# Kernel optimization log

Hardware: AMD Instinct MI355X
Metric: run time of the kernel (lower is better)

## Reference

```python
import jax, jax.numpy as jnp
import numpy as np

B, S = 1, 2048
D = 2048            # n_embd
H = 16              # num heads
KV = 4              # num kv heads
GROUPS = H // KV
D_NOPE = 128
D_ROPE = 64
D_QK = D_NOPE + D_ROPE   # 192
D_V = 128
Q_RANK = 1536
KV_RANK = 512
EPS = 1e-6
MAX_POS = 4096


def rms_norm(x, w, eps=EPS):
    x32 = x.astype(jnp.float32)
    y = x32 * jax.lax.rsqrt(jnp.mean(x32 * x32, axis=-1, keepdims=True) + eps)
    return y.astype(x.dtype) * w


def rotate_half(x):
    x1, x2 = jnp.split(x, 2, axis=-1)
    return jnp.concatenate((-x2, x1), axis=-1)


def setup_inputs() -> dict:
    key = jax.random.key(0)
    ks = jax.random.split(key, 10)
    inv_freq = 1.0 / (10000.0 ** (jnp.arange(0, D_ROPE, 2, dtype=jnp.float32) / D_ROPE))
    t = jnp.arange(MAX_POS, dtype=jnp.float32)
    freqs = jnp.outer(t, inv_freq)                      # [MAX_POS, D_ROPE//2]
    emb = jnp.concatenate((freqs, freqs), axis=-1)      # [MAX_POS, D_ROPE]
    def lin(k, fan_in, fan_out):
        return jax.random.normal(k, (fan_in, fan_out), dtype=jnp.float32) * (fan_in ** -0.5)
    return {
        "hidden_states": jax.random.normal(ks[0], (B, S, D), dtype=jnp.float32),
        "cos": jnp.cos(emb)[None],                      # [1, MAX_POS, D_ROPE]
        "sin": jnp.sin(emb)[None],
        "wq_a": lin(ks[1], D, Q_RANK),
        "q_a_ln_w": jnp.ones((Q_RANK,), jnp.float32),
        "wq_b": lin(ks[2], Q_RANK, H * D_QK),
        "wkv_a": lin(ks[3], D, KV_RANK + D_ROPE),
        "kv_a_ln_w": jnp.ones((KV_RANK,), jnp.float32),
        "wkv_b": lin(ks[4], KV_RANK, KV * (D_NOPE + D_V)),
        "wo": lin(ks[5], H * D_V, D),
        "cache_position": jnp.arange(S, dtype=jnp.int64),
    }


def reference(hidden_states, cos, sin, wq_a, q_a_ln_w, wq_b, wkv_a, kv_a_ln_w,
              wkv_b, wo, cache_position):
    b, s, _ = hidden_states.shape
    # --- query low-rank path ---
    q_a = hidden_states @ wq_a                           # [B,S,Q_RANK]
    q = rms_norm(q_a, q_a_ln_w) @ wq_b                   # [B,S,H*D_QK]
    q = q.reshape(b, s, H, D_QK).transpose(0, 2, 1, 3)   # [B,H,S,D_QK]
    q_pass, q_rot = q[..., :D_NOPE], q[..., D_NOPE:]
    # --- kv low-rank path ---
    ckv = hidden_states @ wkv_a                          # [B,S,KV_RANK+D_ROPE]
    k_pass_a, k_rot_a = ckv[..., :KV_RANK], ckv[..., KV_RANK:]
    kv = rms_norm(k_pass_a, kv_a_ln_w) @ wkv_b           # [B,S,KV*(D_NOPE+D_V)]
    kv = kv.reshape(b, s, KV, D_NOPE + D_V).transpose(0, 2, 1, 3)  # [B,KV,S,*]
    k_pass, v = kv[..., :D_NOPE], kv[..., D_NOPE:]
    # --- partial RoPE ---
    c = cos[0][cache_position][None, None]               # [1,1,S,D_ROPE]
    sn = sin[0][cache_position][None, None]
    q_rot = q_rot * c + rotate_half(q_rot) * sn          # [B,H,S,D_ROPE]
    k_rot = k_rot_a[:, None]                             # [B,1,S,D_ROPE]
    k_rot = k_rot * c + rotate_half(k_rot) * sn
    k_rot = jnp.broadcast_to(k_rot, (b, KV, s, D_ROPE))
    k = jnp.concatenate((k_pass, k_rot), axis=-1)        # [B,KV,S,D_QK]
    # GQA expansion (repeat_interleave over head dim)
    k = jnp.repeat(k, GROUPS, axis=1)                    # [B,H,S,D_QK]
    v = jnp.repeat(v, GROUPS, axis=1)                    # [B,H,S,D_V]
    q_full = jnp.concatenate((q_pass, q_rot), axis=-1)   # [B,H,S,D_QK]
    # causal SDPA (default scale = 1/sqrt(D_QK), matching torch sdpa)
    scale = 1.0 / jnp.sqrt(jnp.float32(D_QK))
    scores = jnp.einsum("bhqd,bhkd->bhqk", q_full, k) * scale
    causal = jnp.tril(jnp.ones((s, s), dtype=bool))
    scores = jnp.where(causal[None, None], scores, jnp.finfo(scores.dtype).min)
    attn = jax.nn.softmax(scores, axis=-1)
    out = jnp.einsum("bhqk,bhkd->bhqd", attn, v)         # [B,H,S,D_V]
    out = out.transpose(0, 2, 1, 3).reshape(b, s, H * D_V)
    return out @ wo                                      # [B,S,D]
```

## Files before the change

kernel.cpp:

```cpp
#include <hip/hip_runtime.h>
#include <hip/hip_bf16.h>


#define S_LEN 2048
#define D_MODEL 2048
#define NH 16
#define NKV 4
#define D_QK 192
#define D_NOPE 128
#define D_ROPE 64
#define D_V 128
#define Q_RANK 1536
#define KV_RANK 512
#define CKV_PITCH 640
#define QDIM (NH * D_QK)
#define KVDIM (NKV * (D_NOPE + D_V))
#define ODIM (NH * D_V)
#define SCALE_QK 0.07216878364870322f
#define SPLIT 2

#define DT_B16 0
#define DT_F32 1
#define DT_AUTO 2

typedef __bf16 bf16x8 __attribute__((ext_vector_type(8)));
typedef float  f32x4  __attribute__((ext_vector_type(4)));
typedef unsigned short u16x8 __attribute__((ext_vector_type(8)));

typedef __attribute__((address_space(1))) const unsigned int as1_u32;
typedef __attribute__((address_space(3))) unsigned int as3_u32;

__device__ __forceinline__ void gl2lds16(const unsigned short* g, unsigned short* l) {
    __builtin_amdgcn_global_load_lds((as1_u32*)g, (as3_u32*)l, 16, 0, 0);
}

__device__ __forceinline__ float b2f(unsigned short u) {
    return __uint_as_float(((unsigned int)u) << 16);
}
__device__ __forceinline__ unsigned short f2b(float f) {
    unsigned int u = __float_as_uint(f);
    return (unsigned short)((u + 0x7fffu + ((u >> 16) & 1u)) >> 16);
}
__device__ __forceinline__ bool flag_f32(const unsigned* dt) {
    return dt[0] == 0x3F800000u;
}
__device__ __forceinline__ bool eff_f32(int mode, bool f32) {
    return mode == DT_F32 || (mode == DT_AUTO && f32);
}
__device__ __forceinline__ float ldany(const void* p, size_t i, bool f32) {
    return f32 ? ((const float*)p)[i] : b2f(((const unsigned short*)p)[i]);
}

__device__ __forceinline__ int xcd_swz(int id, int nwg) {
    return (id & 7) * (nwg >> 3) + (id >> 3);
}

#if __has_builtin(__builtin_amdgcn_mov_dpp)
#define ROR16F(x, n) __int_as_float(__builtin_amdgcn_mov_dpp(__float_as_int(x), 0x120 + (n), 0xf, 0xf, true))
#else
#define ROR16F(x, n) __shfl_xor((x), (n))
#endif

__global__ void __launch_bounds__(256)
prep_k(const void* __restrict__ hs, unsigned short* __restrict__ hsb,
       const void* __restrict__ wq_a, unsigned short* __restrict__ wqaT,
       const void* __restrict__ wkv_a, unsigned short* __restrict__ wkvaT,
       const void* __restrict__ wq_b, unsigned short* __restrict__ wqbT,
       const void* __restrict__ wkv_b, unsigned short* __restrict__ wkvbT,
       const void* __restrict__ wo, unsigned short* __restrict__ woT,
       const unsigned* __restrict__ dt)
{
    const bool f32 = flag_f32(dt);
    const int t = threadIdx.x;
    int id = blockIdx.x;

    if (id < 1024) {
        const int base = id * 4096;
        for (int i = t; i < 4096; i += 256)
            hsb[base + i] = f2b(ldany(hs, base + i, f32));
        return;
    }
    id -= 1024;

    const void* W; unsigned short* WT; int Kdim, Ncols, nkb;
    if (id < 768)        { W = wq_a;  WT = wqaT;  Kdim = D_MODEL; Ncols = Q_RANK;           nkb = 32; }
    else if (id < 1088)  { id -= 768;  W = wkv_a; WT = wkvaT; Kdim = D_MODEL; Ncols = KV_RANK + D_ROPE; nkb = 32; }
    else if (id < 2240)  { id -= 1088; W = wq_b;  WT = wqbT;  Kdim = Q_RANK;  Ncols = QDIM;  nkb = 24; }
    else if (id < 2368)  { id -= 2240; W = wkv_b; WT = wkvbT; Kdim = KV_RANK; Ncols = KVDIM; nkb = 8;  }
    else                 { id -= 2368; W = wo;    WT = woT;   Kdim = ODIM;    Ncols = D_MODEL; nkb = 32; }

    const int k0 = (id % nkb) * 64, n0 = (id / nkb) * 64;

    __shared__ unsigned short tile[64][65];
    for (int i = t; i < 4096; i += 256) {
        int r = i >> 6, c = i & 63;
        float v = (n0 + c < Ncols) ? ldany(W, (size_t)(k0 + r) * Ncols + n0 + c, f32) : 0.f;
        tile[c][r] = f2b(v);
    }
    __syncthreads();
    for (int i = t; i < 4096; i += 256) {
        int nn = i >> 6, kk = i & 63;
        WT[(size_t)(n0 + nn) * Kdim + k0 + kk] = tile[nn][kk];
    }
}

#define SM(BUF, MAT, SUB) (smem + (((BUF) * 4 + (MAT) * 2 + (SUB)) * 4096))

__device__ __forceinline__ void
gemm_core(unsigned short* smem,
          const unsigned short* __restrict__ A, int lda,
          const unsigned short* __restrict__ BT, int ldb, int colB,
          void* __restrict__ C, int ldc, int colC, int K, bool cf, int row0)
{
    const int t = threadIdx.x;
    const int w = t >> 6, lane = t & 63;
    const int half = w >> 2;
    const int wq = w & 3;
    const int wr = wq & 1, wc = wq >> 1;
    const int n = lane & 15, quad = lane >> 4;
    const int e0 = t * 8;
    const int er = e0 >> 5, ec = e0 & 31;

    f32x4 acc[4][4];
#pragma unroll
    for (int i = 0; i < 4; ++i)
#pragma unroll
        for (int j = 0; j < 4; ++j) acc[i][j] = (f32x4){0.f, 0.f, 0.f, 0.f};

#define STAGE(BUF, KB)                                                         \
    do {                                                                       \
        gl2lds16(A  + (size_t)(row0 + er) * lda + (KB) + ec,                   \
                 SM(BUF, 0, 0) + e0);                                          \
        gl2lds16(A  + (size_t)(row0 + er) * lda + (KB) + 32 + ec,              \
                 SM(BUF, 0, 1) + e0);                                          \
        gl2lds16(BT + (size_t)(colB + er) * ldb + (KB) + ec,                   \
                 SM(BUF, 1, 0) + e0);                                          \
        gl2lds16(BT + (size_t)(colB + er) * ldb + (KB) + 32 + ec,              \
                 SM(BUF, 1, 1) + e0);                                          \
    } while (0)

    STAGE(0, 0);

    int cur = 0;
    for (int k0 = 0; k0 < K; k0 += 64) {
        __syncthreads();

        if (k0 + 64 < K) STAGE(cur ^ 1, k0 + 64);

        const unsigned short* Asub = SM(cur, 0, half);
        const unsigned short* Bsub = SM(cur, 1, half);

        bf16x8 af[4], bfr[4];
#pragma unroll
        for (int i = 0; i < 4; ++i)
            af[i] = *(const bf16x8*)&Asub[(wr * 64 + i * 16 + n) * 32 + quad * 8];
#pragma unroll
        for (int j = 0; j < 4; ++j)
            bfr[j] = *(const bf16x8*)&Bsub[(wc * 64 + j * 16 + n) * 32 + quad * 8];
#pragma unroll
        for (int i = 0; i < 4; ++i)
#pragma unroll
            for (int j = 0; j < 4; ++j)
                acc[i][j] = __builtin_amdgcn_mfma_f32_16x16x32_bf16(af[i], bfr[j], acc[i][j], 0, 0, 0);

        cur ^= 1;
    }
#undef STAGE

    __syncthreads();
    float* fsm = (float*)smem;
    if (half == 1) {
        float* dst = fsm + wq * 4096;
#pragma unroll
        for (int i = 0; i < 4; ++i)
#pragma unroll
            for (int j = 0; j < 4; ++j)
#pragma unroll
                for (int r = 0; r < 4; ++r)
                    dst[(i * 16 + quad * 4 + r) * 64 + j * 16 + n] = acc[i][j][r];
    }
    __syncthreads();
    if (half == 0) {
        const float* src = fsm + wq * 4096;
#pragma unroll
        for (int i = 0; i < 4; ++i)
#pragma unroll
            for (int j = 0; j < 4; ++j)
#pragma unroll
                for (int r = 0; r < 4; ++r)
                    acc[i][j][r] += src[(i * 16 + quad * 4 + r) * 64 + j * 16 + n];

#pragma unroll
        for (int i = 0; i < 4; ++i)
#pragma unroll
            for (int r = 0; r < 4; ++r) {
                const int row = row0 + wr * 64 + i * 16 + quad * 4 + r;
                if (cf) {
                    float* crow = (float*)C + (size_t)row * ldc + colC + wc * 64 + n;
#pragma unroll
                    for (int j = 0; j < 4; ++j) crow[j * 16] = acc[i][j][r];
                } else {
                    unsigned short* crow = (unsigned short*)C + (size_t)row * ldc + colC + wc * 64 + n;
#pragma unroll
                    for (int j = 0; j < 4; ++j) crow[j * 16] = f2b(acc[i][j][r]);
                }
            }
    }
}

__global__ void __launch_bounds__(512)
gemm_mfma(const unsigned short* __restrict__ A, int lda,
          const unsigned short* __restrict__ BT, int ldb,
          void* __restrict__ C, int ldc, int K, int cm,
          const unsigned* __restrict__ dt,
          void* __restrict__ C2, int ldc2, int ncol1, int nbx)
{
    __shared__ unsigned short smem[2 * 2 * 2 * 4096];
    const int id = xcd_swz(blockIdx.x, gridDim.x);
    const int bx = id % nbx, by = id / nbx;
    const int row0 = by << 7;
    const int colB = bx << 7;
    void* Cp = C; int ld = ldc; int colC = colB;
    if (colC >= ncol1) { Cp = C2; ld = ldc2; colC -= ncol1; }
    const bool cf = eff_f32(cm, flag_f32(dt));
    gemm_core(smem, A, lda, BT, ldb, colB, Cp, ld, colC, K, cf, row0);
}

__global__ void __launch_bounds__(512)
gemm2_mfma(const unsigned short* __restrict__ A1, int lda1,
           const unsigned short* __restrict__ BT1, int ldb1,
           void* __restrict__ C1, int ldc1, int K1, int nbx1, int nblk1,
           const unsigned short* __restrict__ A2, int lda2,
           const unsigned short* __restrict__ BT2, int ldb2,
           void* __restrict__ C2, int ldc2, int K2, int nbx2)
{
    __shared__ unsigned short smem[2 * 2 * 2 * 4096];
    int id = blockIdx.x;
    if (id < nblk1) {
        id = xcd_swz(id, nblk1);
        const int bx = id % nbx1, by = id / nbx1;
        gemm_core(smem, A1, lda1, BT1, ldb1, bx << 7, C1, ldc1, bx << 7, K1, false, by << 7);
    } else {
        id = xcd_swz(id - nblk1, (int)gridDim.x - nblk1);
        const int bx = id % nbx2, by = id / nbx2;
        gemm_core(smem, A2, lda2, BT2, ldb2, bx << 7, C2, ldc2, bx << 7, K2, false, by << 7);
    }
}

__global__ void __launch_bounds__(256)
rmsnorm2(unsigned short* __restrict__ qa, const void* __restrict__ qw,
         unsigned short* __restrict__ ckvb, const void* __restrict__ kw,
         const unsigned* __restrict__ dt)
{
    const bool f32 = flag_f32(dt);
    const int row = blockIdx.x;
    const int t = threadIdx.x;

    unsigned short* x;
    const void* w;
    int ncols;
    if (row < S_LEN) { x = qa + (size_t)row * Q_RANK; w = qw; ncols = Q_RANK; }
    else             { x = ckvb + (size_t)(row - S_LEN) * CKV_PITCH; w = kw; ncols = KV_RANK; }

    float ss = 0.f;
    for (int i = t; i < ncols; i += 256) { float v = b2f(x[i]); ss += v * v; }
#pragma unroll
    for (int o = 32; o > 0; o >>= 1) ss += __shfl_down(ss, o);

    __shared__ float part[4];
    __shared__ float sc;
    if ((t & 63) == 0) part[t >> 6] = ss;
    __syncthreads();
    if (t == 0) {
        float tot = part[0] + part[1] + part[2] + part[3];
        sc = rsqrtf(tot / (float)ncols + 1e-6f);
    }
    __syncthreads();
    float scale = sc;
    for (int i = t; i < ncols; i += 256)
        x[i] = f2b(b2f(x[i]) * scale * ldany(w, i, f32));
}

__global__ void __launch_bounds__(256)
rope_tv(unsigned short* __restrict__ q, unsigned short* __restrict__ ckvb,
        const void* __restrict__ cosb, const void* __restrict__ sinb,
        const void* __restrict__ cpos,
        const unsigned short* __restrict__ kvb, unsigned short* __restrict__ vt,
        const unsigned* __restrict__ dt)
{
    const int t = threadIdx.x;
    const int bid = blockIdx.x;

    if (bid < S_LEN) {
        const bool f32 = flag_f32(dt);
        const int s = bid;
        const long long* p64 = (const long long*)cpos;
        const int* p32 = (const int*)cpos;
        const bool is64 = (p64[1] == 1LL);
        const int pos = is64 ? (int)p64[s] : p32[s];
        const size_t cb = (size_t)pos * D_ROPE;

        for (int idx = t; idx < NH * 32; idx += 256) {
            int h = idx >> 5, i = idx & 31;
            unsigned short* base = q + (size_t)s * QDIM + h * D_QK + D_NOPE;
            float x1 = b2f(base[i]), x2 = b2f(base[i + 32]);
            float c1 = ldany(cosb, cb + i, f32),      s1 = ldany(sinb, cb + i, f32);
            float c2 = ldany(cosb, cb + i + 32, f32), s2 = ldany(sinb, cb + i + 32, f32);
            base[i]      = f2b(x1 * c1 - x2 * s1);
            base[i + 32] = f2b(x2 * c2 + x1 * s2);
        }
        if (t < 32) {
            int i = t;
            unsigned short* base = ckvb + (size_t)s * CKV_PITCH + KV_RANK;
            float x1 = b2f(base[i]), x2 = b2f(base[i + 32]);
            float c1 = ldany(cosb, cb + i, f32),      s1 = ldany(sinb, cb + i, f32);
            float c2 = ldany(cosb, cb + i + 32, f32), s2 = ldany(sinb, cb + i + 32, f32);
            base[i]      = f2b(x1 * c1 - x2 * s1);
            base[i + 32] = f2b(x2 * c2 + x1 * s2);
        }
        return;
    }

    __shared__ unsigned short tile[64][68];
    const int id2 = bid - S_LEN;
    const int kb = id2 & 31;
    const int yy = id2 >> 5;
    const int kvh = yy >> 1;
    const int d0 = (yy & 1) * 64;

    for (int i = t; i < 64 * 16; i += 256) {
        int r = i >> 4, c4 = (i & 15) << 2;
        ushort4 v = *(const ushort4*)(kvb + (size_t)(kb * 64 + r) * KVDIM
                                      + kvh * 256 + D_NOPE + d0 + c4);
        tile[c4 + 0][r] = v.x;
        tile[c4 + 1][r] = v.y;
        tile[c4 + 2][r] = v.z;
        tile[c4 + 3][r] = v.w;
    }
    __syncthreads();
    for (int i = t; i < 64 * 16; i += 256) {
        int d = i >> 4, k4 = (i & 15) << 2;
        ushort4 v = *(const ushort4*)&tile[d][k4];
        *(ushort4*)(vt + (size_t)(kvh * 128 + d0 + d) * S_LEN + kb * 64 + k4) = v;
    }
}

__global__ void __launch_bounds__(256, 2)
attn_mfma(const unsigned short* __restrict__ q, const unsigned short* __restrict__ kvb,
          const unsigned short* __restrict__ ckvb, const unsigned short* __restrict__ vt,
          unsigned short* __restrict__ pO, float* __restrict__ pm, float* __restrict__ pl)
{
    const int h   = blockIdx.y;
    const int qtb = (int)gridDim.x - 1 - (int)blockIdx.x;
    const int sp  = blockIdx.z;
    const int kvh = h >> 2;
    const int jtmax = 2 * qtb + 1;

    __shared__ unsigned short ks[64][200];
    __shared__ unsigned short vs[128][72];
    __shared__ unsigned short ps[4][2][16][72];

    const int t = threadIdx.x;
    const int w = t >> 6, lane = t & 63;
    const int n = lane & 15, quad = lane >> 4;
    const int qrow0 = qtb * 128 + w * 16;

    bf16x8 qf[2][6];
#pragma unroll
    for (int g = 0; g < 2; ++g) {
        const unsigned short* qrow = q + (size_t)(qrow0 + g * 64 + n) * QDIM + h * D_QK;
#pragma unroll
        for (int s = 0; s < 6; ++s)
            qf[g][s] = *(const bf16x8*)(qrow + s * 32 + quad * 8);
    }

    f32x4 o[2][8];
#pragma unroll
    for (int g = 0; g < 2; ++g)
#pragma unroll
        for (int c = 0; c < 8; ++c) o[g][c] = (f32x4){0.f, 0.f, 0.f, 0.f};
    float mrow[2][4], lrow[2][4];
#pragma unroll
    for (int g = 0; g < 2; ++g)
#pragma unroll
        for (int i = 0; i < 4; ++i) { mrow[g][i] = -3e38f; lrow[g][i] = 0.f; }

    u16x8 kn[4], kr[2], vv[4];

#define PRELOAD(K0)                                                            \
    {                                                                          \
        const int k0_ = (K0);                                                  \
        _Pragma("unroll")                                                      \
        for (int i = 0; i < 4; ++i) {                                          \
            int g = i * 256 + t, r = g >> 4, c = g & 15;                       \
            kn[i] = *(const u16x8*)(kvb + (size_t)(k0_ + r) * KVDIM            \
                                    + kvh * 256 + c * 8);                      \
        }                                                                      \
        _Pragma("unroll")                                                      \
        for (int i = 0; i < 2; ++i) {                                          \
            int g = i * 256 + t, r = g >> 3, c = g & 7;                        \
            kr[i] = *(const u16x8*)(ckvb + (size_t)(k0_ + r) * CKV_PITCH       \
                                    + KV_RANK + c * 8);                        \
        }                                                                      \
        _Pragma("unroll")                                                      \
        for (int i = 0; i < 4; ++i) {                                          \
            int g = i * 256 + t, d = g >> 3, c = g & 7;                        \
            vv[i] = *(const u16x8*)(vt + (size_t)(kvh * 128 + d) * S_LEN       \
                                    + k0_ + c * 8);                            \
        }                                                                      \
    }

    if (sp <= jtmax) PRELOAD(sp << 6);

    for (int jt = sp; jt <= jtmax; jt += SPLIT) {
        __syncthreads();
#pragma unroll
        for (int i = 0; i < 4; ++i) {
            int g = i * 256 + t, r = g >> 4, c = g & 15;
            *(u16x8*)&ks[r][c * 8] = kn[i];
        }
#pragma unroll
        for (int i = 0; i < 2; ++i) {
            int g = i * 256 + t, r = g >> 3, c = g & 7;
            *(u16x8*)&ks[r][128 + c * 8] = kr[i];
        }
#pragma unroll
        for (int i = 0; i < 4; ++i) {
            int g = i * 256 + t, d = g >> 3, c = g & 7;
            *(u16x8*)&vs[d][c * 8] = vv[i];
        }
        __syncthreads();

        if (jt + SPLIT <= jtmax) PRELOAD((jt + SPLIT) << 6);

        const bool act0  = (jt <= 2 * qtb);
        const bool diag0 = (jt == 2 * qtb);
        const bool diag1 = (jt == jtmax);

        f32x4 sf[2][4];
        __builtin_amdgcn_s_setprio(1);
#pragma unroll
        for (int f = 0; f < 4; ++f) {
            f32x4 a0 = (f32x4){0.f, 0.f, 0.f, 0.f};
            f32x4 a1 = (f32x4){0.f, 0.f, 0.f, 0.f};
#pragma unroll
            for (int s = 0; s < 6; ++s) {
                bf16x8 kf = *(const bf16x8*)&ks[f * 16 + n][s * 32 + quad * 8];
                a0 = __builtin_amdgcn_mfma_f32_16x16x32_bf16(qf[0][s], kf, a0, 0, 0, 0);
                a1 = __builtin_amdgcn_mfma_f32_16x16x32_bf16(qf[1][s], kf, a1, 0, 0, 0);
            }
            sf[0][f] = a0; sf[1][f] = a1;
        }
        __builtin_amdgcn_s_setprio(0);

        const bool actg[2]  = {act0, true};
        const bool diagg[2] = {diag0, diag1};

#pragma unroll
        for (int g = 0; g < 2; ++g) {
            if (!actg[g]) continue;
            const bool dg = diagg[g];
#pragma unroll
            for (int f = 0; f < 4; ++f)
#pragma unroll
                for (int i = 0; i < 4; ++i) {
                    float v = sf[g][f][i] * SCALE_QK;
                    if (dg && (f * 16 + n > w * 16 + quad * 4 + i)) v = -3e38f;
                    sf[g][f][i] = v;
                }

            float lmax[4], fac[4], alpha[4], lsum[4];
#pragma unroll
            for (int i = 0; i < 4; ++i)
                lmax[i] = fmaxf(fmaxf(fmaxf(sf[g][0][i], sf[g][1][i]),
                                      fmaxf(sf[g][2][i], sf[g][3][i])), mrow[g][i]);
#pragma unroll
            for (int f = 0; f < 4; ++f)
#pragma unroll
                for (int i = 0; i < 4; ++i)
                    sf[g][f][i] = __expf(sf[g][f][i] - lmax[i]);
#pragma unroll
            for (int i = 0; i < 4; ++i) {
                lsum[i] = (sf[g][0][i] + sf[g][1][i]) + (sf[g][2][i] + sf[g][3][i]);
                float gm = lmax[i];
                gm = fmaxf(gm, ROR16F(gm, 8));
                gm = fmaxf(gm, ROR16F(gm, 4));
                gm = fmaxf(gm, ROR16F(gm, 2));
                gm = fmaxf(gm, ROR16F(gm, 1));
                fac[i]   = __expf(lmax[i] - gm);
                alpha[i] = __expf(mrow[g][i] - gm);
                mrow[g][i] = gm;
                float s = lsum[i] * fac[i];
                s += ROR16F(s, 8);
                s += ROR16F(s, 4);
                s += ROR16F(s, 2);
                s += ROR16F(s, 1);
                lrow[g][i] = lrow[g][i] * alpha[i] + s;
#pragma unroll
                for (int c = 0; c < 8; ++c) o[g][c][i] *= alpha[i];
            }
#pragma unroll
            for (int f = 0; f < 4; ++f)
#pragma unroll
                for (int i = 0; i < 4; ++i)
                    ps[w][g][quad * 4 + i][f * 16 + n] = f2b(sf[g][f][i] * fac[i]);
        }

        __asm__ __volatile__("s_waitcnt lgkmcnt(0)" ::: "memory");

        bf16x8 pa[2][2];
#pragma unroll
        for (int g = 0; g < 2; ++g) {
            if (actg[g]) {
                pa[g][0] = *(const bf16x8*)&ps[w][g][n][quad * 8];
                pa[g][1] = *(const bf16x8*)&ps[w][g][n][32 + quad * 8];
            } else {
                pa[g][0] = (bf16x8)(__bf16)0.f;
                pa[g][1] = (bf16x8)(__bf16)0.f;
            }
        }

        __builtin_amdgcn_s_setprio(1);
#pragma unroll
        for (int c = 0; c < 8; ++c) {
            bf16x8 v0 = *(const bf16x8*)&vs[c * 16 + n][quad * 8];
            bf16x8 v1 = *(const bf16x8*)&vs[c * 16 + n][32 + quad * 8];
            o[0][c] = __builtin_amdgcn_mfma_f32_16x16x32_bf16(pa[0][0], v0, o[0][c], 0, 0, 0);
            o[0][c] = __builtin_amdgcn_mfma_f32_16x16x32_bf16(pa[0][1], v1, o[0][c], 0, 0, 0);
            o[1][c] = __builtin_amdgcn_mfma_f32_16x16x32_bf16(pa[1][0], v0, o[1][c], 0, 0, 0);
            o[1][c] = __builtin_amdgcn_mfma_f32_16x16x32_bf16(pa[1][1], v1, o[1][c], 0, 0, 0);
        }
        __builtin_amdgcn_s_setprio(0);
    }
#undef PRELOAD

#pragma unroll
    for (int g = 0; g < 2; ++g)
#pragma unroll
        for (int i = 0; i < 4; ++i) {
            const int row = qrow0 + g * 64 + quad * 4 + i;
            const size_t slot = ((size_t)(sp * S_LEN + row) * NH + h);
            unsigned short* orow = pO + slot * 128 + n;
#pragma unroll
            for (int c = 0; c < 8; ++c)
                orow[c * 16] = f2b(o[g][c][i]);
            if (n == 0) { pm[slot] = mrow[g][i]; pl[slot] = lrow[g][i]; }
        }
}

__global__ void __launch_bounds__(256)
combine_k(const unsigned short* __restrict__ pO, const float* __restrict__ pm,
          const float* __restrict__ pl, unsigned short* __restrict__ obuf)
{
    const int row = blockIdx.x;
    const int t = threadIdx.x;
    __shared__ float wsc[NH][SPLIT];

    if (t < NH) {
        const int h = t;
        float m[SPLIT], l[SPLIT];
        float mx = -3e38f;
#pragma unroll
        for (int s = 0; s < SPLIT; ++s) {
            const size_t slot = ((size_t)(s * S_LEN + row) * NH + h);
            m[s] = pm[slot]; l[s] = pl[slot];
            mx = fmaxf(mx, m[s]);
        }
        float lsum = 0.f;
#pragma unroll
        for (int s = 0; s < SPLIT; ++s) lsum += __expf(m[s] - mx) * l[s];
        float inv = 1.f / lsum;
#pragma unroll
        for (int s = 0; s < SPLIT; ++s) wsc[h][s] = __expf(m[s] - mx) * inv;
    }
    __syncthreads();

    for (int idx = t; idx < ODIM; idx += 256) {
        const int h = idx >> 7, d = idx & 127;
        float sum = 0.f;
#pragma unroll
        for (int s = 0; s < SPLIT; ++s) {
            const size_t slot = ((size_t)(s * S_LEN + row) * NH + h);
            sum += b2f(pO[slot * 128 + d]) * wsc[h][s];
        }
        obuf[(size_t)row * ODIM + idx] = f2b(sum);
    }
}


extern "C" void kernel_launch(void* const* d_in, const int* in_sizes, int n_in,
                              void* d_out, int out_size, void* d_ws, size_t ws_size,
                              hipStream_t stream)
{
    const void* hs    = d_in[0];
    const void* cosb  = d_in[1];
    const void* sinb  = d_in[2];
    const void* wq_a  = d_in[3];
    const void* q_ln  = d_in[4];
    const void* wq_b  = d_in[5];
    const void* wkv_a = d_in[6];
    const void* kv_ln = d_in[7];
    const void* wkv_b = d_in[8];
    const void* wo    = d_in[9];
    const void* cpos  = d_in[10];
    const unsigned* dt = (const unsigned*)d_in[4];

    char* ws = (char*)d_ws;
    unsigned short* woT   = (unsigned short*)ws; ws += (size_t)D_MODEL * ODIM    * 2;
    unsigned short* ckvb  = (unsigned short*)ws; ws += (size_t)S_LEN * CKV_PITCH * 2;
    unsigned short* qbuf  = (unsigned short*)ws; ws += (size_t)S_LEN * QDIM      * 2;
    unsigned short* kvb   = (unsigned short*)ws; ws += (size_t)S_LEN * KVDIM     * 2;
    unsigned short* vtb   = (unsigned short*)ws; ws += (size_t)NKV * D_V * S_LEN * 2;
    unsigned short* obuf  = (unsigned short*)ws; ws += (size_t)S_LEN * ODIM      * 2;

    char* scratch = ws;
    unsigned short* hsb   = (unsigned short*)scratch;
    unsigned short* wqaT  = hsb   + (size_t)S_LEN * D_MODEL;
    unsigned short* wkvaT = wqaT  + (size_t)Q_RANK * D_MODEL;
    unsigned short* wqbT  = wkvaT + (size_t)CKV_PITCH * D_MODEL;
    unsigned short* wkvbT = wqbT  + (size_t)QDIM * Q_RANK;
    unsigned short* q_a   = wkvbT + (size_t)KVDIM * KV_RANK;
    unsigned short* pO    = (unsigned short*)scratch;
    float*          pm    = (float*)(pO + (size_t)SPLIT * S_LEN * NH * 128);
    float*          pl    = pm + (size_t)SPLIT * S_LEN * NH;

    prep_k<<<4416, 256, 0, stream>>>(hs, hsb, wq_a, wqaT, wkv_a, wkvaT,
                                     wq_b, wqbT, wkv_b, wkvbT, wo, woT, dt);

    gemm_mfma<<<(Q_RANK + CKV_PITCH) / 128 * (S_LEN / 128), 512, 0, stream>>>(
        hsb, D_MODEL, wqaT, D_MODEL, q_a, Q_RANK, D_MODEL, DT_B16, dt,
        ckvb, CKV_PITCH, Q_RANK, (Q_RANK + CKV_PITCH) / 128);

    rmsnorm2<<<2 * S_LEN, 256, 0, stream>>>(q_a, q_ln, ckvb, kv_ln, dt);

    gemm2_mfma<<<(QDIM / 128) * (S_LEN / 128) + (KVDIM / 128) * (S_LEN / 128),
                 512, 0, stream>>>(
        q_a, Q_RANK, wqbT, Q_RANK, qbuf, QDIM, Q_RANK, QDIM / 128,
        (QDIM / 128) * (S_LEN / 128),
        ckvb, CKV_PITCH, wkvbT, KV_RANK, kvb, KVDIM, KV_RANK, KVDIM / 128);

    rope_tv<<<S_LEN + (S_LEN / 64) * 8, 256, 0, stream>>>(
        qbuf, ckvb, cosb, sinb, cpos, kvb, vtb, dt);

    attn_mfma<<<dim3(S_LEN / 128, NH, SPLIT), 256, 0, stream>>>(
        qbuf, kvb, ckvb, vtb, pO, pm, pl);

    combine_k<<<S_LEN, 256, 0, stream>>>(pO, pm, pl, obuf);

    gemm_mfma<<<(D_MODEL / 128) * (S_LEN / 128), 512, 0, stream>>>(
        obuf, ODIM, woT, D_MODEL, d_out, D_MODEL, D_MODEL, DT_AUTO, dt,
        nullptr, 0, 1 << 30, D_MODEL / 128);
}
```

Measured before the change: 335.6 us.

## Use 128x256 output tiles for the q_b/kv_b GEMM pair

Adds a GEMM core that computes 128x256 output tiles: eight waves each hold a 64x64 accumulator and share a staged A tile across two 128-column B halves. The q_b and kv_b projections switch to this core, which halves the block count and the A-tile reloads per output column. In exchange, LDS use per block rises to 96KB, which lowers occupancy and leaves fewer blocks to spread across the GPU's compute units.

```diff
diff --git a/kernel.cpp b/kernel.cpp
--- a/kernel.cpp
+++ b/kernel.cpp
@@ -208,6 +208,88 @@
     }
 }
 
+#define SMA(BUF, KS)        (smem + (((BUF) * 6 + (KS)) * 4096))
+#define SMB(BUF, H128, KS)  (smem + (((BUF) * 6 + 2 + (H128) * 2 + (KS)) * 4096))
+
+__device__ __forceinline__ void
+gemm_big_core(unsigned short* smem,
+              const unsigned short* __restrict__ A, int lda,
+              const unsigned short* __restrict__ BT, int ldb, int colB,
+              unsigned short* __restrict__ C, int ldc, int K, int row0)
+{
+    const int t = threadIdx.x;
+    const int w = t >> 6, lane = t & 63;
+    const int wr = w & 1, wc = w >> 1;
+    const int n = lane & 15, quad = lane >> 4;
+    const int e0 = t * 8;
+    const int er = e0 >> 5, ec = e0 & 31;
+
+    f32x4 acc[4][4];
+#pragma unroll
+    for (int i = 0; i < 4; ++i)
+#pragma unroll
+        for (int j = 0; j < 4; ++j) acc[i][j] = (f32x4){0.f, 0.f, 0.f, 0.f};
+
+#define STAGEB(BUF, KB)                                                        \
+    do {                                                                       \
+        gl2lds16(A + (size_t)(row0 + er) * lda + (KB) + ec,                    \
+                 SMA(BUF, 0) + e0);                                            \
+        gl2lds16(A + (size_t)(row0 + er) * lda + (KB) + 32 + ec,               \
+                 SMA(BUF, 1) + e0);                                            \
+        gl2lds16(BT + (size_t)(colB + er) * ldb + (KB) + ec,                   \
+                 SMB(BUF, 0, 0) + e0);                                         \
+        gl2lds16(BT + (size_t)(colB + er) * ldb + (KB) + 32 + ec,              \
+                 SMB(BUF, 0, 1) + e0);                                         \
+        gl2lds16(BT + (size_t)(colB + 128 + er) * ldb + (KB) + ec,             \
+                 SMB(BUF, 1, 0) + e0);                                         \
+        gl2lds16(BT + (size_t)(colB + 128 + er) * ldb + (KB) + 32 + ec,        \
+                 SMB(BUF, 1, 1) + e0);                                         \
+    } while (0)
+
+    STAGEB(0, 0);
+
+    const int bh   = wc >> 1;
+    const int bloc = (wc & 1) * 64;
+
+    int cur = 0;
+    for (int k0 = 0; k0 < K; k0 += 64) {
+        __syncthreads();
+
+        if (k0 + 64 < K) STAGEB(cur ^ 1, k0 + 64);
+
+#pragma unroll
+        for (int ks = 0; ks < 2; ++ks) {
+            const unsigned short* Asub = SMA(cur, ks);
+            const unsigned short* Bsub = SMB(cur, bh, ks);
+            bf16x8 af[4], bfr[4];
+#pragma unroll
+            for (int i = 0; i < 4; ++i)
+                af[i] = *(const bf16x8*)&Asub[(wr * 64 + i * 16 + n) * 32 + quad * 8];
+#pragma unroll
+            for (int j = 0; j < 4; ++j)
+                bfr[j] = *(const bf16x8*)&Bsub[(bloc + j * 16 + n) * 32 + quad * 8];
+#pragma unroll
+            for (int i = 0; i < 4; ++i)
+#pragma unroll
+                for (int j = 0; j < 4; ++j)
+                    acc[i][j] = __builtin_amdgcn_mfma_f32_16x16x32_bf16(af[i], bfr[j], acc[i][j], 0, 0, 0);
+        }
+
+        cur ^= 1;
+    }
+#undef STAGEB
+
+#pragma unroll
+    for (int i = 0; i < 4; ++i)
+#pragma unroll
+        for (int r = 0; r < 4; ++r) {
+            const int row = row0 + wr * 64 + i * 16 + quad * 4 + r;
+            unsigned short* crow = C + (size_t)row * ldc + colB + wc * 64 + n;
+#pragma unroll
+            for (int j = 0; j < 4; ++j) crow[j * 16] = f2b(acc[i][j][r]);
+        }
+}
+
 __global__ void __launch_bounds__(512)
 gemm_mfma(const unsigned short* __restrict__ A, int lda,
           const unsigned short* __restrict__ BT, int ldb,
@@ -229,21 +311,21 @@
 __global__ void __launch_bounds__(512)
 gemm2_mfma(const unsigned short* __restrict__ A1, int lda1,
            const unsigned short* __restrict__ BT1, int ldb1,
-           void* __restrict__ C1, int ldc1, int K1, int nbx1, int nblk1,
+           unsigned short* __restrict__ C1, int ldc1, int K1, int nbx1, int nblk1,
            const unsigned short* __restrict__ A2, int lda2,
            const unsigned short* __restrict__ BT2, int ldb2,
-           void* __restrict__ C2, int ldc2, int K2, int nbx2)
-{
-    __shared__ unsigned short smem[2 * 2 * 2 * 4096];
+           unsigned short* __restrict__ C2, int ldc2, int K2, int nbx2)
+{
+    __shared__ unsigned short smem[2 * 6 * 4096];
     int id = blockIdx.x;
     if (id < nblk1) {
         id = xcd_swz(id, nblk1);
         const int bx = id % nbx1, by = id / nbx1;
-        gemm_core(smem, A1, lda1, BT1, ldb1, bx << 7, C1, ldc1, bx << 7, K1, false, by << 7);
+        gemm_big_core(smem, A1, lda1, BT1, ldb1, bx << 8, C1, ldc1, K1, by << 7);
     } else {
         id = xcd_swz(id - nblk1, (int)gridDim.x - nblk1);
         const int bx = id % nbx2, by = id / nbx2;
-        gemm_core(smem, A2, lda2, BT2, ldb2, bx << 7, C2, ldc2, bx << 7, K2, false, by << 7);
+        gemm_big_core(smem, A2, lda2, BT2, ldb2, bx << 8, C2, ldc2, K2, by << 7);
     }
 }
 
@@ -633,11 +715,11 @@
 
     rmsnorm2<<<2 * S_LEN, 256, 0, stream>>>(q_a, q_ln, ckvb, kv_ln, dt);
 
-    gemm2_mfma<<<(QDIM / 128) * (S_LEN / 128) + (KVDIM / 128) * (S_LEN / 128),
+    gemm2_mfma<<<(QDIM / 256) * (S_LEN / 128) + (KVDIM / 256) * (S_LEN / 128),
                  512, 0, stream>>>(
-        q_a, Q_RANK, wqbT, Q_RANK, qbuf, QDIM, Q_RANK, QDIM / 128,
-        (QDIM / 128) * (S_LEN / 128),
-        ckvb, CKV_PITCH, wkvbT, KV_RANK, kvb, KVDIM, KV_RANK, KVDIM / 128);
+        q_a, Q_RANK, wqbT, Q_RANK, qbuf, QDIM, Q_RANK, QDIM / 256,
+        (QDIM / 256) * (S_LEN / 128),
+        ckvb, CKV_PITCH, wkvbT, KV_RANK, kvb, KVDIM, KV_RANK, KVDIM / 256);
 
     rope_tv<<<S_LEN + (S_LEN / 64) * 8, 256, 0, stream>>>(
         qbuf, ckvb, cosb, sinb, cpos, kvb, vtb, dt);
```

Result: no change. 336.3 us (+0.2%).
